# Kernel tuning notes

Measured on AMD Instinct MI355X. Metric: run time of the kernel, lower is better.

## Reference

```python
import jax, jax.numpy as jnp
import numpy as np

N = 128        # num nodes == num activities (required by the flatten->linear coupling)
F_IN = 256     # num_node_features
H = 512        # graph_conv_layer_sizes
E = 524288     # number of edges
D0, D1 = 512, 256  # dense_layer_sizes


def _edge_conv(x, src, dst, W1, b1, W2, b2):
    # gather endpoints per edge: x_i = target, x_j = source (PyG source_to_target flow)
    x_i = x[dst]                      # [E, C]
    x_j = x[src]                      # [E, C]
    t = jnp.concatenate([x_i, x_j - x_i], axis=1)          # [E, 2C]
    m = jnp.dot(jax.nn.relu(jnp.dot(t, W1) + b1), W2) + b2  # [E, H]
    agg = jax.ops.segment_max(m, dst, num_segments=N)       # scatter-max into targets
    # PyG fills empty segments with 0; segment_max yields -inf for empty segments
    return jnp.where(jnp.isfinite(agg), agg, 0.0)


def setup_inputs() -> dict:
    key = jax.random.key(0)
    ks = jax.random.split(key, 16)

    def w(k, shape, fan_in):
        return (jax.random.normal(k, shape, jnp.float32) / np.float32(np.sqrt(fan_in)))

    return {
        "x": jax.random.normal(ks[0], (N, F_IN), jnp.float32),
        "edge_index": jax.random.randint(ks[1], (2, E), 0, N, dtype=jnp.int32),
        # EdgeConv 1: Linear(2*F_IN -> H), ReLU, Linear(H -> H)
        "c1_W1": w(ks[2], (2 * F_IN, H), 2 * F_IN), "c1_b1": jnp.zeros((H,), jnp.float32),
        "c1_W2": w(ks[3], (H, H), H),               "c1_b2": jnp.zeros((H,), jnp.float32),
        # EdgeConv 2: Linear(2*H -> H), ReLU, Linear(H -> H)
        "c2_W1": w(ks[4], (2 * H, H), 2 * H),       "c2_b1": jnp.zeros((H,), jnp.float32),
        "c2_W2": w(ks[5], (H, H), H),               "c2_b2": jnp.zeros((H,), jnp.float32),
        # dense head on flattened [N*H] vector
        "lin_W": w(ks[6], (N * H, D0), N * H),      "lin_b": jnp.zeros((D0,), jnp.float32),
        "lin1_W": w(ks[7], (D0, D1), D0),           "lin1_b": jnp.zeros((D1,), jnp.float32),
        "out_W": w(ks[8], (D1, N), D1),             "out_b": jnp.zeros((N,), jnp.float32),
    }


def reference(x, edge_index, c1_W1, c1_b1, c1_W2, c1_b2,
              c2_W1, c2_b1, c2_W2, c2_b2,
              lin_W, lin_b, lin1_W, lin1_b, out_W, out_b):
    src, dst = edge_index[0], edge_index[1]
    h = jax.nn.relu(_edge_conv(x, src, dst, c1_W1, c1_b1, c1_W2, c1_b2))
    h = jax.nn.relu(_edge_conv(h, src, dst, c2_W1, c2_b1, c2_W2, c2_b2))
    v = h.reshape(-1)                       # torch.flatten; dropout is identity in eval
    v = jax.nn.relu(jnp.dot(v, lin_W) + lin_b)
    v = jax.nn.relu(jnp.dot(v, lin1_W) + lin1_b)
    v = jax.nn.relu(jnp.dot(v, out_W) + out_b)
    return jax.nn.softmax(v, axis=0)
```

## Files before the change

### kernel.cpp

```cpp
#include <hip/hip_runtime.h>
#include <cfloat>
#include <cmath>
#include <cstdint>

#define N_NODES 128
#define F_IN    256
#define HDIM    512
#define NEDGE   524288
#define NREP    32

typedef _Float16 half8 __attribute__((ext_vector_type(8)));
typedef _Float16 half4 __attribute__((ext_vector_type(4)));
typedef float f32x4 __attribute__((ext_vector_type(4)));

template <int KK, int S>
__device__ __forceinline__ void uv_body(
    const float* __restrict__ A, const float* __restrict__ W,
    const float* __restrict__ bias, float* __restrict__ U,
    float* __restrict__ V, const int h0, const int ks0, const bool addb,
    char* smem) {
  constexpr int KS = KK / S;
  constexpr int BK = 32;
  float(*As)[BK + 1] = (float(*)[BK + 1])smem;
  float(*Wd)[20] = (float(*)[20])(smem + 128 * (BK + 1) * 4);
  float(*Wb)[20] = (float(*)[20])(smem + 128 * (BK + 1) * 4 + BK * 20 * 4);
  const int t = threadIdx.x;
  const int tx = t & 3;
  const int ty = t >> 2;

  float accU[2][4], accV[2][4];
#pragma unroll
  for (int i = 0; i < 2; ++i)
#pragma unroll
    for (int j = 0; j < 4; ++j) { accU[i][j] = 0.f; accV[i][j] = 0.f; }

  for (int ch = 0; ch < KS / BK; ++ch) {
    const int k0 = ks0 + ch * BK;
    __syncthreads();
#pragma unroll
    for (int i = 0; i < 4; ++i) {
      const int slot = t + i * 256;
      const int dd = slot >> 3, kw = (slot & 7) * 4;
      const float4 a4 =
          *reinterpret_cast<const float4*>(&A[dd * KK + k0 + kw]);
      As[dd][kw + 0] = a4.x;
      As[dd][kw + 1] = a4.y;
      As[dd][kw + 2] = a4.z;
      As[dd][kw + 3] = a4.w;
    }
    if (t < 128) {
      const int k = t >> 2, hq = (t & 3) * 4;
      const float4 wt = *reinterpret_cast<const float4*>(
          &W[(size_t)(k0 + k) * HDIM + h0 + hq]);
      const float4 wb = *reinterpret_cast<const float4*>(
          &W[(size_t)(KK + k0 + k) * HDIM + h0 + hq]);
      *reinterpret_cast<float4*>(&Wb[k][hq]) = wb;
      float4 wd;
      wd.x = wt.x - wb.x; wd.y = wt.y - wb.y;
      wd.z = wt.z - wb.z; wd.w = wt.w - wb.w;
      *reinterpret_cast<float4*>(&Wd[k][hq]) = wd;
    }
    __syncthreads();
#pragma unroll
    for (int k = 0; k < BK; ++k) {
      float a[2];
#pragma unroll
      for (int i = 0; i < 2; ++i) a[i] = As[ty * 2 + i][k];
      const float4 wd4 = *reinterpret_cast<const float4*>(&Wd[k][tx * 4]);
      const float4 wb4 = *reinterpret_cast<const float4*>(&Wb[k][tx * 4]);
      const float wdv[4] = {wd4.x, wd4.y, wd4.z, wd4.w};
      const float wbv[4] = {wb4.x, wb4.y, wb4.z, wb4.w};
#pragma unroll
      for (int i = 0; i < 2; ++i)
#pragma unroll
        for (int j = 0; j < 4; ++j) {
          accU[i][j] = fmaf(a[i], wdv[j], accU[i][j]);
          accV[i][j] = fmaf(a[i], wbv[j], accV[i][j]);
        }
    }
  }
  const int cbase = h0 + tx * 4;
  float bb[4] = {0.f, 0.f, 0.f, 0.f};
  if (addb) {
#pragma unroll
    for (int j = 0; j < 4; ++j) bb[j] = bias[cbase + j];
  }
#pragma unroll
  for (int i = 0; i < 2; ++i) {
    const int row = ty * 2 + i;
#pragma unroll
    for (int j = 0; j < 4; ++j) {
      atomicAdd(&U[row * HDIM + cbase + j], accU[i][j] + bb[j]);
      atomicAdd(&V[row * HDIM + cbase + j], accV[i][j]);
    }
  }
}

__global__ __launch_bounds__(256) void prep_uv1_kernel(
    const int* __restrict__ ei, unsigned int* __restrict__ mask,
    const float* __restrict__ W2a, const float* __restrict__ W2b,
    _Float16* __restrict__ Ta, _Float16* __restrict__ Tb,
    const float* __restrict__ x, const float* __restrict__ W1,
    const float* __restrict__ b1, float* __restrict__ U1,
    float* __restrict__ V1) {
  __shared__ __align__(16) char smem[22016];
  const int bx = blockIdx.x;
  const int t = threadIdx.x;
  if (bx < 128) {
    const int hx = bx & 31, ky = bx >> 5;
    uv_body<F_IN, 4>(x, W1, b1, U1, V1, hx * 16, ky * (F_IN / 4),
                     ky == 0, smem);
  } else if (bx < 384) {
    unsigned int* lm = (unsigned int*)smem;
    for (int i = t; i < N_NODES * 4; i += 256) lm[i] = 0u;
    __syncthreads();
    const int base = (bx - 128) * 2048;
#pragma unroll
    for (int r = 0; r < 8; ++r) {
      const int e = base + r * 256 + t;
      const int s = ei[e];
      const int d = ei[NEDGE + e];
      atomicOr(&lm[d * 4 + (s >> 5)], 1u << (s & 31));
    }
    __syncthreads();
    for (int i = t; i < N_NODES * 4; i += 256) {
      const unsigned int v = lm[i];
      if (v) atomicOr(&mask[i], v);
    }
  } else {
    const int b = bx - 384;
    const int layer = b >> 6;
    const int rem = b & 63;
    const int kb = (rem & 7) * 64;
    const int nb = (rem >> 3) * 64;
    const float* W = layer ? W2b : W2a;
    _Float16* T = layer ? Tb : Ta;
    _Float16(*tile)[72] = (_Float16(*)[72])smem;
#pragma unroll
    for (int i = 0; i < 4; ++i) {
      const int slot = t + i * 256;
      const int kk = slot >> 4;
      const int nq = (slot & 15) * 4;
      const float4 w4 = *reinterpret_cast<const float4*>(
          &W[(size_t)(kb + kk) * HDIM + nb + nq]);
      tile[nq + 0][kk] = (_Float16)w4.x;
      tile[nq + 1][kk] = (_Float16)w4.y;
      tile[nq + 2][kk] = (_Float16)w4.z;
      tile[nq + 3][kk] = (_Float16)w4.w;
    }
    __syncthreads();
#pragma unroll
    for (int i = 0; i < 2; ++i) {
      const int slot = t + i * 256;
      const int n = slot >> 3;
      const int ko = (slot & 7) * 8;
      *reinterpret_cast<half8*>(&T[(size_t)(nb + n) * HDIM + kb + ko]) =
          *reinterpret_cast<const half8*>(&tile[n][ko]);
    }
  }
}

template <int KK, int S>
__global__ __launch_bounds__(256) void uv_gemm_kernel(
    const float* __restrict__ A, const float* __restrict__ W,
    const float* __restrict__ bias, float* __restrict__ U,
    float* __restrict__ V) {
  __shared__ __align__(16) char smem[22016];
  uv_body<KK, S>(A, W, bias, U, V, blockIdx.x * 16, blockIdx.y * (KK / S),
                 blockIdx.y == 0, smem);
}

#define PBK 64
__global__ __launch_bounds__(256) void pair_mfma_kernel(
    const float* __restrict__ U, const float* __restrict__ V,
    const _Float16* __restrict__ W2t, const float* __restrict__ b2,
    const unsigned int* __restrict__ mask, float* __restrict__ out) {
  __shared__ __align__(16) _Float16 As[128][PBK + 8];
  __shared__ _Float16 Bs[128][PBK + 8];
  __shared__ float Ur[HDIM];
  __shared__ float red[4][128];
  const int t = threadIdx.x;
  const int d = blockIdx.y;
  const int c0 = blockIdx.x * 128;
  const int lane = t & 63;
  const int wid = t >> 6;
  const int l15 = lane & 15;
  const int quad = lane >> 4;

  for (int i = t; i < HDIM; i += 256) Ur[i] = U[d * HDIM + i];
  const unsigned int mwv[4] = {mask[d * 4 + 0], mask[d * 4 + 1],
                               mask[d * 4 + 2], mask[d * 4 + 3]};

  f32x4 acc[8][2];
#pragma unroll
  for (int mt = 0; mt < 8; ++mt)
#pragma unroll
    for (int nt = 0; nt < 2; ++nt) acc[mt][nt] = (f32x4)(0.f);

  for (int ch = 0; ch < HDIM / PBK; ++ch) {
    const int k0 = ch * PBK;
    __syncthreads();
#pragma unroll
    for (int i = 0; i < 8; ++i) {
      const int slot = t + i * 256;
      const int s = slot >> 4;
      const int kq = (slot & 15) * 4;
      const float4 v4 =
          *reinterpret_cast<const float4*>(&V[s * HDIM + k0 + kq]);
      const float4 u4 = *reinterpret_cast<const float4*>(&Ur[k0 + kq]);
      half4 h;
      h.x = (_Float16)fmaxf(u4.x + v4.x, 0.f);
      h.y = (_Float16)fmaxf(u4.y + v4.y, 0.f);
      h.z = (_Float16)fmaxf(u4.z + v4.z, 0.f);
      h.w = (_Float16)fmaxf(u4.w + v4.w, 0.f);
      *reinterpret_cast<half4*>(&As[s][kq]) = h;
    }
#pragma unroll
    for (int i = 0; i < 4; ++i) {
      const int slot = t + i * 256;
      const int n = slot >> 3;
      const int ko = (slot & 7) * 8;
      *reinterpret_cast<half8*>(&Bs[n][ko]) = *reinterpret_cast<const half8*>(
          &W2t[(size_t)(c0 + n) * HDIM + k0 + ko]);
    }
    __syncthreads();
#pragma unroll
    for (int ks = 0; ks < PBK / 32; ++ks) {
      half8 bf[2];
#pragma unroll
      for (int nt = 0; nt < 2; ++nt)
        bf[nt] = *reinterpret_cast<const half8*>(
            &Bs[wid * 32 + nt * 16 + l15][ks * 32 + quad * 8]);
#pragma unroll
      for (int mt = 0; mt < 8; ++mt) {
        const half8 af = *reinterpret_cast<const half8*>(
            &As[mt * 16 + l15][ks * 32 + quad * 8]);
#pragma unroll
        for (int nt = 0; nt < 2; ++nt)
          acc[mt][nt] = __builtin_amdgcn_mfma_f32_16x16x32_f16(
              af, bf[nt], acc[mt][nt], 0, 0, 0);
      }
    }
  }
  __syncthreads();
#pragma unroll
  for (int nt = 0; nt < 2; ++nt) {
    float pm = -FLT_MAX;
#pragma unroll
    for (int mt = 0; mt < 8; ++mt) {
      const int sbase = mt * 16 + quad * 4;
      const unsigned int w = mwv[sbase >> 5] >> (sbase & 31);
#pragma unroll
      for (int r = 0; r < 4; ++r)
        if ((w >> r) & 1u) pm = fmaxf(pm, acc[mt][nt][r]);
    }
    red[quad][wid * 32 + nt * 16 + l15] = pm;
  }
  __syncthreads();
  if (t < 128) {
    const float m = fmaxf(fmaxf(red[0][t], red[1][t]),
                          fmaxf(red[2][t], red[3][t]));
    out[d * HDIM + c0 + t] = fmaxf(m + b2[c0 + t], 0.f);
  }
}

__global__ __launch_bounds__(256) void head_gemv5_kernel(
    const float* __restrict__ v, const float* __restrict__ W,
    float* __restrict__ z0r) {
  __shared__ float vs[64];
  __shared__ float red[4][512];
  const int t = threadIdx.x;
  const int b = blockIdx.x;
  const int r0 = b * 64;
  if (t < 64) vs[t] = v[r0 + t];
  __syncthreads();
  const int w = t >> 6;
  const int l = t & 63;
  const float* Wp = W + (size_t)(r0 + w * 16) * 512 + l * 8;
  float4 accA = make_float4(0.f, 0.f, 0.f, 0.f);
  float4 accB = make_float4(0.f, 0.f, 0.f, 0.f);
#pragma unroll
  for (int bb = 0; bb < 2; ++bb) {
    float4 wa[8], wb[8];
#pragma unroll
    for (int i = 0; i < 8; ++i) {
      const float* p = Wp + (size_t)(bb * 8 + i) * 512;
      wa[i] = *reinterpret_cast<const float4*>(p);
      wb[i] = *reinterpret_cast<const float4*>(p + 4);
    }
#pragma unroll
    for (int i = 0; i < 8; ++i) {
      const float xv = vs[w * 16 + bb * 8 + i];
      accA.x = fmaf(xv, wa[i].x, accA.x);
      accA.y = fmaf(xv, wa[i].y, accA.y);
      accA.z = fmaf(xv, wa[i].z, accA.z);
      accA.w = fmaf(xv, wa[i].w, accA.w);
      accB.x = fmaf(xv, wb[i].x, accB.x);
      accB.y = fmaf(xv, wb[i].y, accB.y);
      accB.z = fmaf(xv, wb[i].z, accB.z);
      accB.w = fmaf(xv, wb[i].w, accB.w);
    }
  }
  *reinterpret_cast<float4*>(&red[w][l * 8]) = accA;
  *reinterpret_cast<float4*>(&red[w][l * 8 + 4]) = accB;
  __syncthreads();
  float* zr = z0r + (size_t)(b & (NREP - 1)) * 512;
  const float s0 = red[0][t] + red[1][t] + red[2][t] + red[3][t];
  const int c2 = t + 256;
  const float s1 = red[0][c2] + red[1][c2] + red[2][c2] + red[3][c2];
  atomicAdd(&zr[t], s0);
  atomicAdd(&zr[c2], s1);
}

__global__ __launch_bounds__(512) void head_tail_kernel(
    const float* __restrict__ z0r, const float* __restrict__ lin_b,
    const float* __restrict__ lin1W, const float* __restrict__ lin1b,
    const float* __restrict__ outW, const float* __restrict__ outb,
    float* __restrict__ out) {
  __shared__ float zr[512];
  __shared__ float r1[2][256];
  __shared__ float z1s[256];
  __shared__ float r2[4][128];
  __shared__ float z2s[128];
  __shared__ float rr[128];
  const int t = threadIdx.x;
  {
    float s = 0.f;
#pragma unroll
    for (int r = 0; r < NREP; ++r) s += z0r[r * 512 + t];
    zr[t] = fmaxf(s + lin_b[t], 0.f);
  }
  __syncthreads();
  {
    const int c = t & 255;
    const int kh = t >> 8;
    float acc = 0.f;
#pragma unroll
    for (int b2 = 0; b2 < 16; ++b2) {
      const int k0 = kh * 256 + b2 * 16;
      float wv[16];
#pragma unroll
      for (int i = 0; i < 16; ++i) wv[i] = lin1W[(size_t)(k0 + i) * 256 + c];
#pragma unroll
      for (int i = 0; i < 16; ++i) acc = fmaf(zr[k0 + i], wv[i], acc);
    }
    r1[kh][c] = acc;
  }
  __syncthreads();
  if (t < 256) z1s[t] = fmaxf(r1[0][t] + r1[1][t] + lin1b[t], 0.f);
  __syncthreads();
  {
    const int c = t & 127;
    const int kq = t >> 7;
    float acc = 0.f;
#pragma unroll
    for (int b2 = 0; b2 < 4; ++b2) {
      const int k0 = kq * 64 + b2 * 16;
      float wv[16];
#pragma unroll
      for (int i = 0; i < 16; ++i) wv[i] = outW[(size_t)(k0 + i) * 128 + c];
#pragma unroll
      for (int i = 0; i < 16; ++i) acc = fmaf(z1s[k0 + i], wv[i], acc);
    }
    r2[kq][c] = acc;
  }
  __syncthreads();
  if (t < 128) {
    const float z =
        fmaxf(r2[0][t] + r2[1][t] + r2[2][t] + r2[3][t] + outb[t], 0.f);
    z2s[t] = z;
    rr[t] = z;
  }
  __syncthreads();
  for (int off = 64; off > 0; off >>= 1) {
    if (t < off) rr[t] = fmaxf(rr[t], rr[t + off]);
    __syncthreads();
  }
  const float mx = rr[0];
  __syncthreads();
  if (t < 128) {
    const float e = expf(z2s[t] - mx);
    z2s[t] = e;
    rr[t] = e;
  }
  __syncthreads();
  for (int off = 64; off > 0; off >>= 1) {
    if (t < off) rr[t] += rr[t + off];
    __syncthreads();
  }
  if (t < 128) out[t] = z2s[t] / rr[0];
}

extern "C" void kernel_launch(void* const* d_in, const int* in_sizes, int n_in,
                              void* d_out, int out_size, void* d_ws,
                              size_t ws_size, hipStream_t stream) {
  const float* x      = (const float*)d_in[0];
  const int*   ei     = (const int*)d_in[1];
  const float* c1_W1  = (const float*)d_in[2];
  const float* c1_b1  = (const float*)d_in[3];
  const float* c1_W2  = (const float*)d_in[4];
  const float* c1_b2  = (const float*)d_in[5];
  const float* c2_W1  = (const float*)d_in[6];
  const float* c2_b1  = (const float*)d_in[7];
  const float* c2_W2  = (const float*)d_in[8];
  const float* c2_b2  = (const float*)d_in[9];
  const float* lin_W  = (const float*)d_in[10];
  const float* lin_b  = (const float*)d_in[11];
  const float* lin1_W = (const float*)d_in[12];
  const float* lin1_b = (const float*)d_in[13];
  const float* out_W  = (const float*)d_in[14];
  const float* out_b  = (const float*)d_in[15];
  float* out = (float*)d_out;

  char* wsb = (char*)d_ws;
  unsigned int* mask = (unsigned int*)wsb;
  float* z0r = (float*)(wsb + 2048);
  float* U1 = z0r + NREP * 512;
  float* V1 = U1 + 65536;
  float* U2 = V1 + 65536;
  float* V2 = U2 + 65536;
  const size_t zero_bytes = 2048 + (size_t)NREP * 512 * 4 + 4 * 65536 * 4;
  float* h1 = V2 + 65536;
  float* h2 = h1 + 65536;
  _Float16* W2t1 = (_Float16*)(h2 + 65536);
  _Float16* W2t2 = W2t1 + 262144;

  hipMemsetAsync(wsb, 0, zero_bytes, stream);
  prep_uv1_kernel<<<512, 256, 0, stream>>>(ei, mask, c1_W2, c2_W2, W2t1, W2t2,
                                           x, c1_W1, c1_b1, U1, V1);
  pair_mfma_kernel<<<dim3(4, 128), 256, 0, stream>>>(U1, V1, W2t1, c1_b2,
                                                     mask, h1);
  uv_gemm_kernel<512, 8><<<dim3(32, 8), 256, 0, stream>>>(h1, c2_W1, c2_b1,
                                                          U2, V2);
  pair_mfma_kernel<<<dim3(4, 128), 256, 0, stream>>>(U2, V2, W2t2, c2_b2,
                                                     mask, h2);
  head_gemv5_kernel<<<1024, 256, 0, stream>>>(h2, lin_W, z0r);
  head_tail_kernel<<<1, 512, 0, stream>>>(z0r, lin_b, lin1_W, lin1_b, out_W,
                                          out_b, out);
}
```

Before: 307.4 us.

## Prefetch lin_W into cache with extra blocks in earlier kernels

Adds dedicated streaming blocks to the prep, pair-MFMA and second UV-GEMM launches. Each streaming block reads a slice of the 128 MB lin_W matrix and discards the result, so the whole matrix is touched before the head GEMV runs. The aim is to overlap the bandwidth-bound head weight read with the earlier compute-bound graph-conv stages, so the head kernel hits the large last-level cache instead of HBM. The risks are that the extra blocks compete with the useful blocks for compute units and bandwidth, and that the gain depends on the data staying resident in cache.

```diff
diff --git a/kernel.cpp b/kernel.cpp
--- a/kernel.cpp
+++ b/kernel.cpp
@@ -12,6 +12,26 @@
 typedef _Float16 half8 __attribute__((ext_vector_type(8)));
 typedef _Float16 half4 __attribute__((ext_vector_type(4)));
 typedef float f32x4 __attribute__((ext_vector_type(4)));
+
+__device__ __forceinline__ void stream_rows(const float* __restrict__ W,
+                                            long r0, int nrows) {
+  const f32x4* p = reinterpret_cast<const f32x4*>(W + (size_t)r0 * 512);
+  const int n4 = nrows * 128;
+  const int t = threadIdx.x;
+  f32x4 acc = (f32x4)(0.f);
+  for (int i = t; i < n4; i += 2048) {
+    f32x4 v0 = p[i];
+    f32x4 v1 = p[i + 256];
+    f32x4 v2 = p[i + 512];
+    f32x4 v3 = p[i + 768];
+    f32x4 v4 = p[i + 1024];
+    f32x4 v5 = p[i + 1280];
+    f32x4 v6 = p[i + 1536];
+    f32x4 v7 = p[i + 1792];
+    acc += ((v0 + v1) + (v2 + v3)) + ((v4 + v5) + (v6 + v7));
+  }
+  asm volatile("" ::"v"(acc.x), "v"(acc.y), "v"(acc.z), "v"(acc.w));
+}
 
 template <int KK, int S>
 __device__ __forceinline__ void uv_body(
@@ -102,19 +122,24 @@
     _Float16* __restrict__ Ta, _Float16* __restrict__ Tb,
     const float* __restrict__ x, const float* __restrict__ W1,
     const float* __restrict__ b1, float* __restrict__ U1,
-    float* __restrict__ V1) {
+    float* __restrict__ V1, const float* __restrict__ linW) {
   __shared__ __align__(16) char smem[22016];
   const int bx = blockIdx.x;
   const int t = threadIdx.x;
-  if (bx < 128) {
-    const int hx = bx & 31, ky = bx >> 5;
+  if ((bx % 5) == 4) {
+    stream_rows(linW, (long)(bx / 5) * 96, 96);
+    return;
+  }
+  const int fi = bx - (bx + 1) / 5;
+  if (fi < 128) {
+    const int hx = fi & 31, ky = fi >> 5;
     uv_body<F_IN, 4>(x, W1, b1, U1, V1, hx * 16, ky * (F_IN / 4),
                      ky == 0, smem);
-  } else if (bx < 384) {
+  } else if (fi < 384) {
     unsigned int* lm = (unsigned int*)smem;
     for (int i = t; i < N_NODES * 4; i += 256) lm[i] = 0u;
     __syncthreads();
-    const int base = (bx - 128) * 2048;
+    const int base = (fi - 128) * 2048;
 #pragma unroll
     for (int r = 0; r < 8; ++r) {
       const int e = base + r * 256 + t;
@@ -128,7 +153,7 @@
       if (v) atomicOr(&mask[i], v);
     }
   } else {
-    const int b = bx - 384;
+    const int b = fi - 384;
     const int layer = b >> 6;
     const int rem = b & 63;
     const int kb = (rem & 7) * 64;
@@ -164,24 +189,37 @@
 __global__ __launch_bounds__(256) void uv_gemm_kernel(
     const float* __restrict__ A, const float* __restrict__ W,
     const float* __restrict__ bias, float* __restrict__ U,
-    float* __restrict__ V) {
+    float* __restrict__ V, const float* __restrict__ linW, long sbase) {
   __shared__ __align__(16) char smem[22016];
-  uv_body<KK, S>(A, W, bias, U, V, blockIdx.x * 16, blockIdx.y * (KK / S),
-                 blockIdx.y == 0, smem);
+  const int bx = blockIdx.x;
+  if ((bx % 3) == 2) {
+    stream_rows(linW, sbase + (long)(bx / 3) * 96, 96);
+    return;
+  }
+  const int fi = bx - (bx + 1) / 3;
+  uv_body<KK, S>(A, W, bias, U, V, (fi & 31) * 16, (fi >> 5) * (KK / S),
+                 (fi >> 5) == 0, smem);
 }
 
 #define PBK 64
 __global__ __launch_bounds__(256) void pair_mfma_kernel(
     const float* __restrict__ U, const float* __restrict__ V,
     const _Float16* __restrict__ W2t, const float* __restrict__ b2,
-    const unsigned int* __restrict__ mask, float* __restrict__ out) {
+    const unsigned int* __restrict__ mask, float* __restrict__ out,
+    const float* __restrict__ linW, long sbase) {
   __shared__ __align__(16) _Float16 As[128][PBK + 8];
   __shared__ _Float16 Bs[128][PBK + 8];
   __shared__ float Ur[HDIM];
   __shared__ float red[4][128];
-  const int t = threadIdx.x;
-  const int d = blockIdx.y;
-  const int c0 = blockIdx.x * 128;
+  const int bx = blockIdx.x;
+  if ((bx % 5) == 4) {
+    stream_rows(linW, sbase + (long)(bx / 5) * 160, 160);
+    return;
+  }
+  const int fi = bx - (bx + 1) / 5;
+  const int t = threadIdx.x;
+  const int d = fi >> 2;
+  const int c0 = (fi & 3) * 128;
   const int lane = t & 63;
   const int wid = t >> 6;
   const int l15 = lane & 15;
@@ -248,8 +286,8 @@
     float pm = -FLT_MAX;
 #pragma unroll
     for (int mt = 0; mt < 8; ++mt) {
-      const int sbase = mt * 16 + quad * 4;
-      const unsigned int w = mwv[sbase >> 5] >> (sbase & 31);
+      const int sbase2 = mt * 16 + quad * 4;
+      const unsigned int w = mwv[sbase2 >> 5] >> (sbase2 & 31);
 #pragma unroll
       for (int r = 0; r < 4; ++r)
         if ((w >> r) & 1u) pm = fmaxf(pm, acc[mt][nt][r]);
@@ -426,14 +464,14 @@
   _Float16* W2t2 = W2t1 + 262144;
 
   hipMemsetAsync(wsb, 0, zero_bytes, stream);
-  prep_uv1_kernel<<<512, 256, 0, stream>>>(ei, mask, c1_W2, c2_W2, W2t1, W2t2,
-                                           x, c1_W1, c1_b1, U1, V1);
-  pair_mfma_kernel<<<dim3(4, 128), 256, 0, stream>>>(U1, V1, W2t1, c1_b2,
-                                                     mask, h1);
-  uv_gemm_kernel<512, 8><<<dim3(32, 8), 256, 0, stream>>>(h1, c2_W1, c2_b1,
-                                                          U2, V2);
-  pair_mfma_kernel<<<dim3(4, 128), 256, 0, stream>>>(U2, V2, W2t2, c2_b2,
-                                                     mask, h2);
+  prep_uv1_kernel<<<640, 256, 0, stream>>>(ei, mask, c1_W2, c2_W2, W2t1, W2t2,
+                                           x, c1_W1, c1_b1, U1, V1, lin_W);
+  pair_mfma_kernel<<<640, 256, 0, stream>>>(U1, V1, W2t1, c1_b2, mask, h1,
+                                            lin_W, 12288);
+  uv_gemm_kernel<512, 8><<<384, 256, 0, stream>>>(h1, c2_W1, c2_b1, U2, V2,
+                                                  lin_W, 32768);
+  pair_mfma_kernel<<<640, 256, 0, stream>>>(U2, V2, W2t2, c2_b2, mask, h2,
+                                            lin_W, 45056);
   head_gemv5_kernel<<<1024, 256, 0, stream>>>(h2, lin_W, z0r);
   head_tail_kernel<<<1, 512, 0, stream>>>(z0r, lin_b, lin1_W, lin1_b, out_W,
                                           out_b, out);
```

After: 324.9 us. 5.7% more time.
